# Optimization experiments

Measured on AMD Instinct MI355X. Metric: run time of the kernel, lower is better.

Reference implementation:

```python
import jax, jax.numpy as jnp
import numpy as np

NUM_ATOM_TYPES = 28   # ZINC-Full atom vocab
HIDDEN_DIM = 128
N_ATOMS = 500_000
N_INCIDENCES = 2_000_000
NUM_CYCLES = 500_000  # static segment count for scatter_sum output


def setup_inputs() -> dict:
    key = jax.random.key(0)
    k1, k2, k3 = jax.random.split(key, 3)
    x = jax.random.randint(k1, (N_ATOMS,), 0, NUM_ATOM_TYPES, dtype=jnp.int64)
    atom_to_cycle = jax.random.randint(
        k2, (2, N_INCIDENCES), 0, NUM_CYCLES, dtype=jnp.int64)
    # row 0 must index into x's N_ATOMS rows; NUM_CYCLES == N_ATOMS so in-range.
    emb_weight = jax.random.normal(k3, (NUM_ATOM_TYPES, HIDDEN_DIM), dtype=jnp.float32)
    return {"x": x, "atom_to_cycle": atom_to_cycle, "emb_weight": emb_weight}


def reference(x, atom_to_cycle, emb_weight):
    # Embedding lookup: [N_ATOMS, H]
    h = emb_weight[x]
    # Gather per-incidence atom embeddings: [E, H]
    gathered = h[atom_to_cycle[0]]
    # scatter_sum over cycle ids -> [NUM_CYCLES, H]
    return jax.ops.segment_sum(gathered, atom_to_cycle[1], num_segments=NUM_CYCLES)
```

## Files before the change

kernel.cpp:

```cpp
#include <hip/hip_runtime.h>
#include <string.h>

#define H 128
#define NTYPES 28
#define CNT_BYTES_PER_CYCLE 32

__global__ void count_kernel(const int* __restrict__ a2c,
                             const int* __restrict__ x,
                             unsigned* __restrict__ cnt,
                             int n_inc) {
    int i = (blockIdx.x * blockDim.x + threadIdx.x) * 4;
    if (i + 3 < n_inc) {
        int4 at = *(const int4*)(a2c + i);
        int4 cy = *(const int4*)(a2c + n_inc + i);
        int t0 = x[at.x], t1 = x[at.y], t2 = x[at.z], t3 = x[at.w];
        atomicAdd(&cnt[cy.x * 8 + (t0 >> 2)], 1u << (8 * (t0 & 3)));
        atomicAdd(&cnt[cy.y * 8 + (t1 >> 2)], 1u << (8 * (t1 & 3)));
        atomicAdd(&cnt[cy.z * 8 + (t2 >> 2)], 1u << (8 * (t2 & 3)));
        atomicAdd(&cnt[cy.w * 8 + (t3 >> 2)], 1u << (8 * (t3 & 3)));
    } else {
        for (int e = i; e < n_inc; ++e) {
            int atom = a2c[e];
            int cycv = a2c[n_inc + e];
            int t = x[atom];
            atomicAdd(&cnt[cycv * 8 + (t >> 2)], 1u << (8 * (t & 3)));
        }
    }
}

__global__ __launch_bounds__(256) void expand_kernel(
        const unsigned char* __restrict__ cnt,
        const float* __restrict__ emb,
        float* __restrict__ out,
        int num_cycles) {
    __shared__ __align__(16) float lds[NTYPES * H];
    for (int i = threadIdx.x; i < NTYPES * H; i += blockDim.x) lds[i] = emb[i];
    __syncthreads();
    const float2* l2 = (const float2*)lds;

    int lane = threadIdx.x & 63;
    int w    = blockIdx.x * (blockDim.x >> 6) + (threadIdx.x >> 6);
    int nw   = gridDim.x * (blockDim.x >> 6);

    for (int c = w; c < num_cycles; c += nw) {
        unsigned b = cnt[(size_t)c * CNT_BYTES_PER_CYCLE + (lane & 31)];
        unsigned long long m = __ballot(b != 0) & 0x0FFFFFFFull;
        float2 acc = {0.f, 0.f};
        while (m) {
            int t = __builtin_ctzll(m);
            m &= m - 1;
            float f = (float)__builtin_amdgcn_readlane((int)b, t);
            float2 wv = l2[t * 64 + lane];
            acc.x += f * wv.x;
            acc.y += f * wv.y;
        }
        unsigned long long bits;
        memcpy(&bits, &acc, 8);
        __builtin_nontemporal_store(
            bits, (unsigned long long*)(out + (size_t)c * H) + lane);
    }
}

__global__ void scatter_direct_kernel(const int* __restrict__ a2c,
                                      const int* __restrict__ x,
                                      const float* __restrict__ emb,
                                      float* __restrict__ out,
                                      int n_inc) {
    int gid = blockIdx.x * blockDim.x + threadIdx.x;
    int e  = gid >> 5;
    int ch = gid & 31;
    if (e >= n_inc) return;
    int atom = a2c[e];
    int cyc  = a2c[n_inc + e];
    int t    = x[atom];
    const float4 w = ((const float4*)(emb + t * H))[ch];
    float* o = out + (size_t)cyc * H + ch * 4;
    atomicAdd(o + 0, w.x);
    atomicAdd(o + 1, w.y);
    atomicAdd(o + 2, w.z);
    atomicAdd(o + 3, w.w);
}

__global__ void zero_u4_kernel(uint4* __restrict__ p, int n4) {
    int i = blockIdx.x * blockDim.x + threadIdx.x;
    if (i < n4) p[i] = make_uint4(0u, 0u, 0u, 0u);
}

extern "C" void kernel_launch(void* const* d_in, const int* in_sizes, int n_in,
                              void* d_out, int out_size, void* d_ws, size_t ws_size,
                              hipStream_t stream) {
    const int*   x    = (const int*)d_in[0];
    const int*   a2c  = (const int*)d_in[1];
    const float* emb  = (const float*)d_in[2];
    float*       out  = (float*)d_out;

    const int n_inc      = in_sizes[1] / 2;
    const int num_cycles = out_size / H;
    const size_t cnt_bytes = (size_t)num_cycles * CNT_BYTES_PER_CYCLE;

    if (ws_size >= cnt_bytes) {
        unsigned* cnt = (unsigned*)d_ws;
        hipMemsetAsync(d_ws, 0, cnt_bytes, stream);
        int nthreads = (n_inc + 3) / 4;
        count_kernel<<<(nthreads + 255) / 256, 256, 0, stream>>>(a2c, x, cnt, n_inc);
        expand_kernel<<<2048, 256, 0, stream>>>(
            (const unsigned char*)cnt, emb, out, num_cycles);
    } else {
        int n4 = out_size / 4;
        zero_u4_kernel<<<(n4 + 255) / 256, 256, 0, stream>>>((uint4*)d_out, n4);
        long long total = (long long)n_inc * 32;
        int blocks = (int)((total + 255) / 256);
        scatter_direct_kernel<<<blocks, 256, 0, stream>>>(a2c, x, emb, out, n_inc);
    }
}
```

Measured before the change: 364.1 us.

## Bin incidences by cycle bucket and build histograms in shared memory

Replaces the direct global atomic histogram with a two-pass scheme. Incidence keys (cycle, type) are first appended into per-bucket arrays of 512 cycles each, with an overflow list for full buckets. Each bucket's packed byte counts are then built with LDS atomics and written out densely, which also removes the 16MB memset of the count buffer. The cost is extra global traffic for the key bins, contended atomic appends on the bucket counters, and two additional kernel launches.

```diff
diff --git a/kernel.cpp b/kernel.cpp
--- a/kernel.cpp
+++ b/kernel.cpp
@@ -4,6 +4,88 @@
 #define H 128
 #define NTYPES 28
 #define CNT_BYTES_PER_CYCLE 32
+
+#define BKT_SHIFT 9
+#define BKT_CYCLES (1 << BKT_SHIFT)
+#define BKT_CAP 3072
+
+#define OFF_BINCNT 0
+#define OFF_OVFCNT 4096
+#define OFF_BINS   8192
+
+__device__ __forceinline__ void push_key(unsigned key,
+                                         unsigned* __restrict__ bins,
+                                         unsigned* __restrict__ bincnt,
+                                         unsigned* __restrict__ ovf,
+                                         unsigned* __restrict__ ovfcnt) {
+    unsigned b = key >> (5 + BKT_SHIFT);
+    unsigned pos = atomicAdd(&bincnt[b], 1u);
+    if (pos < BKT_CAP) bins[(size_t)b * BKT_CAP + pos] = key;
+    else               ovf[atomicAdd(ovfcnt, 1u)] = key;
+}
+
+__global__ void scatter_bin_kernel(const int* __restrict__ a2c,
+                                   const int* __restrict__ x,
+                                   unsigned* __restrict__ bins,
+                                   unsigned* __restrict__ bincnt,
+                                   unsigned* __restrict__ ovf,
+                                   unsigned* __restrict__ ovfcnt,
+                                   int n_inc) {
+    int i = (blockIdx.x * blockDim.x + threadIdx.x) * 4;
+    if (i + 3 < n_inc) {
+        int4 at = *(const int4*)(a2c + i);
+        int4 cy = *(const int4*)(a2c + n_inc + i);
+        int t0 = x[at.x], t1 = x[at.y], t2 = x[at.z], t3 = x[at.w];
+        push_key(((unsigned)cy.x << 5) | (unsigned)t0, bins, bincnt, ovf, ovfcnt);
+        push_key(((unsigned)cy.y << 5) | (unsigned)t1, bins, bincnt, ovf, ovfcnt);
+        push_key(((unsigned)cy.z << 5) | (unsigned)t2, bins, bincnt, ovf, ovfcnt);
+        push_key(((unsigned)cy.w << 5) | (unsigned)t3, bins, bincnt, ovf, ovfcnt);
+    } else {
+        for (int e = i; e < n_inc; ++e) {
+            unsigned key = ((unsigned)a2c[n_inc + e] << 5) | (unsigned)x[a2c[e]];
+            push_key(key, bins, bincnt, ovf, ovfcnt);
+        }
+    }
+}
+
+__global__ __launch_bounds__(256) void bucket_hist_kernel(
+        const unsigned* __restrict__ bins,
+        const unsigned* __restrict__ bincnt,
+        unsigned* __restrict__ cnt,
+        int num_cycles) {
+    __shared__ unsigned h[BKT_CYCLES * 8];
+    int b = blockIdx.x;
+    for (int j = threadIdx.x; j < BKT_CYCLES * 8; j += blockDim.x) h[j] = 0;
+    __syncthreads();
+    unsigned n = bincnt[b];
+    if (n > BKT_CAP) n = BKT_CAP;
+    const unsigned* mybin = bins + (size_t)b * BKT_CAP;
+    for (unsigned k = threadIdx.x; k < n; k += blockDim.x) {
+        unsigned key   = mybin[k];
+        unsigned local = (key >> 5) & (BKT_CYCLES - 1);
+        unsigned t     = key & 31u;
+        atomicAdd(&h[local * 8 + (t >> 2)], 1u << (8 * (t & 3)));
+    }
+    __syncthreads();
+    int base_dw = b * BKT_CYCLES * 8;
+    int ndw = BKT_CYCLES * 8;
+    int lim = num_cycles * 8 - base_dw;
+    if (lim < ndw) ndw = lim;
+    for (int j = threadIdx.x; j < ndw; j += blockDim.x)
+        cnt[(size_t)base_dw + j] = h[j];
+}
+
+__global__ void ovf_apply_kernel(const unsigned* __restrict__ ovf,
+                                 const unsigned* __restrict__ ovfcnt,
+                                 unsigned* __restrict__ cnt) {
+    unsigned n = *ovfcnt;
+    for (unsigned k = blockIdx.x * blockDim.x + threadIdx.x; k < n;
+         k += gridDim.x * blockDim.x) {
+        unsigned key = ovf[k];
+        unsigned cy = key >> 5, t = key & 31u;
+        atomicAdd(&cnt[(size_t)cy * 8 + (t >> 2)], 1u << (8 * (t & 3)));
+    }
+}
 
 __global__ void count_kernel(const int* __restrict__ a2c,
                              const int* __restrict__ x,
@@ -98,7 +180,30 @@
     const int num_cycles = out_size / H;
     const size_t cnt_bytes = (size_t)num_cycles * CNT_BYTES_PER_CYCLE;
 
-    if (ws_size >= cnt_bytes) {
+    const int    nb         = (num_cycles + BKT_CYCLES - 1) >> BKT_SHIFT;
+    const size_t bins_bytes = (size_t)nb * BKT_CAP * 4;
+    const size_t ovf_bytes  = (size_t)n_inc * 4;
+    const size_t off_ovf    = OFF_BINS + bins_bytes;
+    const size_t off_cnt    = (off_ovf + ovf_bytes + 255) & ~(size_t)255;
+    const size_t need       = off_cnt + cnt_bytes;
+
+    if (ws_size >= need && (size_t)nb * 4 <= OFF_OVFCNT) {
+        char* w = (char*)d_ws;
+        unsigned* bincnt = (unsigned*)(w + OFF_BINCNT);
+        unsigned* ovfcnt = (unsigned*)(w + OFF_OVFCNT);
+        unsigned* bins   = (unsigned*)(w + OFF_BINS);
+        unsigned* ovf    = (unsigned*)(w + off_ovf);
+        unsigned* cnt    = (unsigned*)(w + off_cnt);
+
+        hipMemsetAsync(w, 0, OFF_BINS, stream);
+        int nthreads = (n_inc + 3) / 4;
+        scatter_bin_kernel<<<(nthreads + 255) / 256, 256, 0, stream>>>(
+            a2c, x, bins, bincnt, ovf, ovfcnt, n_inc);
+        bucket_hist_kernel<<<nb, 256, 0, stream>>>(bins, bincnt, cnt, num_cycles);
+        ovf_apply_kernel<<<256, 256, 0, stream>>>(ovf, ovfcnt, cnt);
+        expand_kernel<<<2048, 256, 0, stream>>>(
+            (const unsigned char*)cnt, emb, out, num_cycles);
+    } else if (ws_size >= cnt_bytes) {
         unsigned* cnt = (unsigned*)d_ws;
         hipMemsetAsync(d_ws, 0, cnt_bytes, stream);
         int nthreads = (n_inc + 3) / 4;
```

Result: slower. 701.6 us (+92.7%).

## Process two cycles per wave with float4 lanes and prefetched counts

Applied to the files above, without the earlier changes.

The expand kernel now has each wavefront handle a pair of cycles, one per 32-lane half. Each lane writes a 16-byte vector, and each wave works through a contiguous block of cycle pairs instead of striding across all cycles. Count bytes for the next two pairs are loaded ahead of use to hide their global-memory latency. In exchange, the per-half type loops can diverge, and readlane is replaced by a cross-lane shuffle (__shfl) that has to go through LDS.

```diff
diff --git a/kernel.cpp b/kernel.cpp
--- a/kernel.cpp
+++ b/kernel.cpp
@@ -4,6 +4,8 @@
 #define H 128
 #define NTYPES 28
 #define CNT_BYTES_PER_CYCLE 32
+
+typedef float f32x4 __attribute__((ext_vector_type(4)));
 
 __global__ void count_kernel(const int* __restrict__ a2c,
                              const int* __restrict__ x,
@@ -28,7 +30,7 @@
     }
 }
 
-__global__ __launch_bounds__(256) void expand_kernel(
+__global__ __launch_bounds__(256) void expand2_kernel(
         const unsigned char* __restrict__ cnt,
         const float* __restrict__ emb,
         float* __restrict__ out,
@@ -36,28 +38,45 @@
     __shared__ __align__(16) float lds[NTYPES * H];
     for (int i = threadIdx.x; i < NTYPES * H; i += blockDim.x) lds[i] = emb[i];
     __syncthreads();
-    const float2* l2 = (const float2*)lds;
+    const f32x4* l4 = (const f32x4*)lds;
 
-    int lane = threadIdx.x & 63;
-    int w    = blockIdx.x * (blockDim.x >> 6) + (threadIdx.x >> 6);
-    int nw   = gridDim.x * (blockDim.x >> 6);
+    const int lane = threadIdx.x & 63;
+    const int half = lane >> 5;
+    const int hl   = lane & 31;
+    const int w    = blockIdx.x * (blockDim.x >> 6) + (threadIdx.x >> 6);
+    const int nw   = gridDim.x * (blockDim.x >> 6);
 
-    for (int c = w; c < num_cycles; c += nw) {
-        unsigned b = cnt[(size_t)c * CNT_BYTES_PER_CYCLE + (lane & 31)];
-        unsigned long long m = __ballot(b != 0) & 0x0FFFFFFFull;
-        float2 acc = {0.f, 0.f};
+    const int P   = (num_cycles + 1) >> 1;
+    const int ppw = (P + nw - 1) / nw;
+    int p0 = w * ppw;
+    int p1 = p0 + ppw; if (p1 > P) p1 = P;
+    if (p0 >= p1) return;
+
+    unsigned b0 = cnt[(size_t)p0 * 64 + lane];
+    unsigned b1 = (p0 + 1 < p1) ? cnt[(size_t)(p0 + 1) * 64 + lane] : 0u;
+
+    for (int p = p0; p < p1; ++p) {
+        unsigned b = b0;
+        b0 = b1;
+        b1 = (p + 2 < p1) ? cnt[(size_t)(p + 2) * 64 + lane] : 0u;
+
+        int c = 2 * p + half;
+        unsigned long long bal = __ballot(b != 0);
+        unsigned m = (half ? (unsigned)(bal >> 32) : (unsigned)bal) & 0x0FFFFFFFu;
+        if (c >= num_cycles) m = 0;
+
+        f32x4 acc = {0.f, 0.f, 0.f, 0.f};
         while (m) {
-            int t = __builtin_ctzll(m);
+            int t = __builtin_ctz(m);
             m &= m - 1;
-            float f = (float)__builtin_amdgcn_readlane((int)b, t);
-            float2 wv = l2[t * 64 + lane];
-            acc.x += f * wv.x;
-            acc.y += f * wv.y;
+            float f = (float)(unsigned)__shfl((int)b, t + (half << 5));
+            f32x4 wv = l4[t * 32 + hl];
+            acc += f * wv;
         }
-        unsigned long long bits;
-        memcpy(&bits, &acc, 8);
-        __builtin_nontemporal_store(
-            bits, (unsigned long long*)(out + (size_t)c * H) + lane);
+        if (c < num_cycles) {
+            f32x4* dst = (f32x4*)(out + (size_t)c * H) + hl;
+            __builtin_nontemporal_store(acc, dst);
+        }
     }
 }
 
@@ -103,7 +122,7 @@
         hipMemsetAsync(d_ws, 0, cnt_bytes, stream);
         int nthreads = (n_inc + 3) / 4;
         count_kernel<<<(nthreads + 255) / 256, 256, 0, stream>>>(a2c, x, cnt, n_inc);
-        expand_kernel<<<2048, 256, 0, stream>>>(
+        expand2_kernel<<<2048, 256, 0, stream>>>(
             (const unsigned char*)cnt, emb, out, num_cycles);
     } else {
         int n4 = out_size / 4;
```

Measured after the change: 365.4 us. About the same (+0.4%).
